# Kernel optimization log

Hardware: AMD Instinct MI355X
Metric: run time of the kernel (lower is better)

Reference implementation:

```python
import jax, jax.numpy as jnp
import numpy as np

N_NODES = 50000
N_EDGES = 600000
N_GRAPHS = 500
IN_DIM = 64
LATENT = [128, 128, 128]
N_CLASSES = 10
N_PROTO_PER_CLASS = 5
N_PROTO = N_CLASSES * N_PROTO_PER_CLASS
GRAPH_SIZE = 10
PROTO_DIM = LATENT[-1]  # single 'mean' readout
EPS = 1e-4


def setup_inputs() -> dict:
    key = jax.random.key(0)
    ks = jax.random.split(key, 12)
    x = jax.random.normal(ks[0], (N_NODES, IN_DIM), dtype=jnp.float32)
    edge_index = jax.random.randint(ks[1], (2, N_EDGES), 0, N_NODES, dtype=jnp.int64)
    batch = jnp.sort(jax.random.randint(ks[2], (N_NODES,), 0, N_GRAPHS, dtype=jnp.int64))
    # GCN layer params (glorot-ish scaling)
    def lin(k, din, dout):
        s = (6.0 / (din + dout)) ** 0.5
        return jax.random.uniform(k, (din, dout), jnp.float32, -s, s)
    W0 = lin(ks[3], IN_DIM, LATENT[0]); b0 = jnp.zeros((LATENT[0],), jnp.float32)
    W1 = lin(ks[4], LATENT[0], LATENT[1]); b1 = jnp.zeros((LATENT[1],), jnp.float32)
    W2 = lin(ks[5], LATENT[1], LATENT[2]); b2 = jnp.zeros((LATENT[2],), jnp.float32)
    s = (6.0 / (GRAPH_SIZE + PROTO_DIM)) ** 0.5
    proto_node_emb = jax.random.uniform(ks[6], (N_PROTO, GRAPH_SIZE, PROTO_DIM), jnp.float32, -s, s)
    # last layer: +1 on correct-class connections, -0.5 on incorrect (set_last_layer_incorrect_connection)
    proto_class = jnp.arange(N_PROTO) // N_PROTO_PER_CLASS  # [P]
    ident = (proto_class[None, :] == jnp.arange(N_CLASSES)[:, None]).astype(jnp.float32)  # [C,P]
    last_w = ident * 1.0 + (1.0 - ident) * (-0.5)
    return {"x": x, "edge_index": edge_index, "batch": batch,
            "W0": W0, "b0": b0, "W1": W1, "b1": b1, "W2": W2, "b2": b2,
            "proto_node_emb": proto_node_emb, "last_w": last_w}


def _gcn_forward(x, edge_index, batch, W0, b0, W1, b1, W2, b2, proto_node_emb, last_w):
    src, dst = edge_index[0], edge_index[1]
    # symmetric normalization with self-loops: deg_i = 1 + in_degree(i)
    deg = 1.0 + jax.ops.segment_sum(jnp.ones((N_EDGES,), jnp.float32), dst, num_segments=N_NODES)
    dis = jax.lax.rsqrt(deg)  # [N]
    norm = dis[src] * dis[dst]  # [E]

    def gcn_layer(h, W, b):
        hw = h @ W  # [N,d]
        agg = jax.ops.segment_sum(hw[src] * norm[:, None], dst, num_segments=N_NODES)
        agg = agg + hw * (dis * dis)[:, None]  # self-loop contribution (norm = 1/deg)
        return agg + b

    h = jax.nn.relu(gcn_layer(x, W0, b0))
    h = jax.nn.relu(gcn_layer(h, W1, b1))
    h = jax.nn.relu(gcn_layer(h, W2, b2))  # node_emb [N, 128]

    # mean readout per graph
    counts = jax.ops.segment_sum(jnp.ones((N_NODES,), jnp.float32), batch, num_segments=N_GRAPHS)
    gsum = jax.ops.segment_sum(h, batch, num_segments=N_GRAPHS)
    graph_emb = gsum / jnp.maximum(counts, 1.0)[:, None]  # [B, 128]

    # prototype graph embeddings via mean readout over prototype nodes
    proto_graph = proto_node_emb.mean(axis=1)  # [P, 128]

    # squared L2 distances [B, P]
    d2 = (jnp.sum(graph_emb ** 2, axis=1)[:, None]
          + jnp.sum(proto_graph ** 2, axis=1)[None, :]
          - 2.0 * graph_emb @ proto_graph.T)
    d2 = jnp.maximum(d2, 0.0)
    sim = jnp.log((d2 + 1.0) / (d2 + EPS))  # [B, P]

    logits = sim @ last_w.T  # [B, C]
    return logits


def reference(x, edge_index, batch, W0, b0, W1, b1, W2, b2, proto_node_emb, last_w):
    return _gcn_forward(x, edge_index, batch, W0, b0, W1, b1, W2, b2, proto_node_emb, last_w)
```

## Files before the change

### kernel.cpp

```cpp
#include <hip/hip_runtime.h>
#include <hip/hip_fp16.h>

#define N_NODES   50000
#define N_EDGES   600000
#define N_GRAPHS  500
#define IN_DIM    64
#define D         128
#define N_CLASSES 10
#define N_PROTO   50
#define GRAPH_SZ  10
#define EPS_F     1e-4f
#define NC4       (N_NODES * IN_DIM / 4)
#define GRP8      ((N_NODES + 7) / 8)
#define G16_TILES (N_NODES / 16)
#define BKT       64
#define NCB       196
#define CBCAP     4096
#define HBLK      392
#define EPB       ((N_EDGES + HBLK - 1) / HBLK)
#define KPT       ((EPB + 255) / 256)

typedef _Float16 half4_t __attribute__((ext_vector_type(4)));
typedef _Float16 half8_t __attribute__((ext_vector_type(8)));
typedef float    f32x4   __attribute__((ext_vector_type(4)));

struct Params {
    const float* x; const int* esrc; const int* edst; const int* bat;
    const float* W0; const float* b0; const float* W1; const float* b1;
    const float* W2; const float* b2; const float* pe; const float* lw;
    float* out;
    _Float16 *bufA, *bufB, *xs, *Bp0, *Bp1, *Bp2;
    float *pg;
    int *src_sorted, *indeg, *coarse, *cursor;
};

__device__ __forceinline__ float dis_of(const int* __restrict__ indeg, int n) {
    return rsqrtf(1.0f + (float)indeg[n]);
}

__device__ __forceinline__ void pack_one(const float* __restrict__ W,
                                         _Float16* __restrict__ Bp, int nks, int t) {
    int j = t & 7, l = (t >> 3) & 63;
    int rest = t >> 9;
    int s = rest % nks, c = rest / nks;
    int k = s * 32 + (l >> 4) * 8 + j;
    int col = c * 16 + (l & 15);
    Bp[t] = (_Float16)W[k * D + col];
}

__global__ void kw_p0(Params P) {
    int i = blockIdx.x * 256 + threadIdx.x;
    if (i < NCB) { P.cursor[i] = 0; return; }
    i -= NCB;
    if (i < 8192)  { pack_one(P.W0, P.Bp0, IN_DIM / 32, i); return; }
    i -= 8192;
    if (i < 16384) { pack_one(P.W1, P.Bp1, D / 32, i); return; }
    i -= 16384;
    if (i < 16384) { pack_one(P.W2, P.Bp2, D / 32, i); return; }
    i -= 16384;
    if (i < N_PROTO * D) {
        int p = i >> 7, j = i & 127;
        float s = 0.f;
#pragma unroll
        for (int g = 0; g < GRAPH_SZ; ++g) s += P.pe[((size_t)p * GRAPH_SZ + g) * D + j];
        P.pg[i] = s * (1.0f / GRAPH_SZ);
        return;
    }
    i -= N_PROTO * D;
    if (i < NC4) {
        float4 v = ((const float4*)P.x)[i];
        half4_t h = { (_Float16)v.x, (_Float16)v.y, (_Float16)v.z, (_Float16)v.w };
        ((half4_t*)P.xs)[i] = h;
    }
}

__global__ __launch_bounds__(256) void kw_hist(Params P) {
    __shared__ int hcnt[NCB];
    __shared__ int hbase[NCB];
    int tid = threadIdx.x;
    for (int i = tid; i < NCB; i += 256) hcnt[i] = 0;
    __syncthreads();
    int e0 = blockIdx.x * EPB;
    int e1 = e0 + EPB; if (e1 > N_EDGES) e1 = N_EDGES;
    int lr[KPT], pb[KPT], pl[KPT];
#pragma unroll
    for (int i = 0; i < KPT; ++i) {
        int e = e0 + i * 256 + tid;
        lr[i] = -1;
        if (e < e1) {
            int d = P.edst[e];
            int b = d >> 8;
            pb[i] = b;
            pl[i] = P.esrc[e] | ((d & 255) << 16);
            lr[i] = atomicAdd(&hcnt[b], 1);
        }
    }
    __syncthreads();
    for (int i = tid; i < NCB; i += 256)
        hbase[i] = hcnt[i] ? atomicAdd(&P.cursor[i], hcnt[i]) : 0;
    __syncthreads();
#pragma unroll
    for (int i = 0; i < KPT; ++i) {
        if (lr[i] >= 0) {
            int pos = hbase[pb[i]] + lr[i];
            if (pos < CBCAP) P.coarse[(pb[i] << 12) + pos] = pl[i];
        }
    }
}

__global__ __launch_bounds__(256) void kw_sort(Params P) {
    __shared__ int edges[CBCAP];
    __shared__ int nrank[256];
    int b = blockIdx.x, tid = threadIdx.x;
    int total = P.cursor[b]; if (total > CBCAP) total = CBCAP;
    for (int i = tid; i < total; i += 256) edges[i] = P.coarse[(b << 12) + i];
    nrank[tid] = 0;
    __syncthreads();
    for (int i = tid; i < total; i += 256) {
        int pl = edges[i];
        int dl = pl >> 16;
        int r = atomicAdd(&nrank[dl], 1);
        if (r < BKT) P.src_sorted[(((b << 8) | dl) << 6) + r] = pl & 0xFFFF;
    }
    __syncthreads();
    int node = (b << 8) + tid;
    if (node < N_NODES) P.indeg[node] = nrank[tid];
}

__global__ __launch_bounds__(256, 8) void kw_a0g01(Params P) {
    __shared__ _Float16 xa_t[16][72];
    __shared__ _Float16 h1_t[16][136];
    int tid = threadIdx.x;
    int row0 = blockIdx.x * 16;
    int grp = tid >> 5, lane16 = tid & 15, hf = (tid >> 4) & 1;
    int j4 = lane16 * 4;

#pragma unroll
    for (int iter = 0; iter < 2; ++iter) {
        int nrel = iter * 8 + grp;
        int node = row0 + nrel;
        int cnt = P.indeg[node];
        int base = node << 6;
        float a0 = 0.f, a1 = 0.f, a2 = 0.f, a3 = 0.f;
        int k = hf;
        if (k < cnt) {
            int sc = P.src_sorted[base + k];
            float dc = dis_of(P.indeg, sc);
            half4_t vc = *(const half4_t*)&P.xs[(size_t)sc * IN_DIM + j4];
            for (k += 2; k < cnt; k += 2) {
                int sn = P.src_sorted[base + k];
                float dn = dis_of(P.indeg, sn);
                half4_t vn = *(const half4_t*)&P.xs[(size_t)sn * IN_DIM + j4];
                a0 = fmaf((float)vc[0], dc, a0);
                a1 = fmaf((float)vc[1], dc, a1);
                a2 = fmaf((float)vc[2], dc, a2);
                a3 = fmaf((float)vc[3], dc, a3);
                vc = vn; dc = dn;
            }
            a0 = fmaf((float)vc[0], dc, a0);
            a1 = fmaf((float)vc[1], dc, a1);
            a2 = fmaf((float)vc[2], dc, a2);
            a3 = fmaf((float)vc[3], dc, a3);
        }
        a0 += __shfl_xor(a0, 16);
        a1 += __shfl_xor(a1, 16);
        a2 += __shfl_xor(a2, 16);
        a3 += __shfl_xor(a3, 16);
        if (hf == 0) {
            half4_t hv = *(const half4_t*)&P.xs[(size_t)node * IN_DIM + j4];
            float dd = rsqrtf(1.0f + (float)cnt);
            half4_t r = { (_Float16)((fmaf((float)hv[0], dd, a0)) * dd),
                          (_Float16)((fmaf((float)hv[1], dd, a1)) * dd),
                          (_Float16)((fmaf((float)hv[2], dd, a2)) * dd),
                          (_Float16)((fmaf((float)hv[3], dd, a3)) * dd) };
            *(half4_t*)&xa_t[nrel][j4] = r;
        }
    }
    __syncthreads();

    int wave = tid >> 6, lane = tid & 63;
    int l15 = lane & 15;
    int kof = (lane >> 4) * 8;
    int rb  = (lane >> 4) * 4;
    {
        half8_t af0 = *(const half8_t*)&xa_t[l15][kof];
        half8_t af1 = *(const half8_t*)&xa_t[l15][32 + kof];
        f32x4 acc[2];
        acc[0] = (f32x4){0.f, 0.f, 0.f, 0.f};
        acc[1] = (f32x4){0.f, 0.f, 0.f, 0.f};
#pragma unroll
        for (int cc = 0; cc < 2; ++cc) {
            int c = wave * 2 + cc;
            half8_t b0f = *(const half8_t*)&P.Bp0[(size_t)((c * 2 + 0) * 64 + lane) * 8];
            half8_t b1f = *(const half8_t*)&P.Bp0[(size_t)((c * 2 + 1) * 64 + lane) * 8];
            acc[cc] = __builtin_amdgcn_mfma_f32_16x16x32_f16(af0, b0f, acc[cc], 0, 0, 0);
            acc[cc] = __builtin_amdgcn_mfma_f32_16x16x32_f16(af1, b1f, acc[cc], 0, 0, 0);
        }
#pragma unroll
        for (int cc = 0; cc < 2; ++cc) {
            int col = (wave * 2 + cc) * 16 + l15;
            float bv = P.b0[col];
#pragma unroll
            for (int r = 0; r < 4; ++r)
                h1_t[rb + r][col] = (_Float16)fmaxf(acc[cc][r] + bv, 0.f);
        }
    }
    __syncthreads();

    {
        half8_t af[4];
#pragma unroll
        for (int s = 0; s < 4; ++s)
            af[s] = *(const half8_t*)&h1_t[l15][s * 32 + kof];
        f32x4 acc[2];
        acc[0] = (f32x4){0.f, 0.f, 0.f, 0.f};
        acc[1] = (f32x4){0.f, 0.f, 0.f, 0.f};
#pragma unroll
        for (int cc = 0; cc < 2; ++cc) {
            int c = wave * 2 + cc;
#pragma unroll
            for (int s = 0; s < 4; ++s) {
                half8_t bf = *(const half8_t*)&P.Bp1[(size_t)((c * 4 + s) * 64 + lane) * 8];
                acc[cc] = __builtin_amdgcn_mfma_f32_16x16x32_f16(af[s], bf, acc[cc], 0, 0, 0);
            }
        }
        float dsc[4];
#pragma unroll
        for (int r = 0; r < 4; ++r) dsc[r] = dis_of(P.indeg, row0 + rb + r);
#pragma unroll
        for (int cc = 0; cc < 2; ++cc) {
            int col = (wave * 2 + cc) * 16 + l15;
#pragma unroll
            for (int r = 0; r < 4; ++r)
                P.bufA[(size_t)(row0 + rb + r) * D + col] = (_Float16)(acc[cc][r] * dsc[r]);
        }
    }
}

__global__ __launch_bounds__(256, 8) void kw_g1g2(Params P) {
    __shared__ _Float16 h2_t[16][136];
    int tid = threadIdx.x;
    int row0 = blockIdx.x * 16;
    int grp = tid >> 5, lane16 = tid & 15, hf = (tid >> 4) & 1;
    int j8 = lane16 * 8;

#pragma unroll
    for (int iter = 0; iter < 2; ++iter) {
        int nrel = iter * 8 + grp;
        int node = row0 + nrel;
        int cnt = P.indeg[node];
        int base = node << 6;
        float a[8] = {0.f, 0.f, 0.f, 0.f, 0.f, 0.f, 0.f, 0.f};
        int k = hf;
        if (k < cnt) {
            int sc = P.src_sorted[base + k];
            half8_t vc = *(const half8_t*)&P.bufA[(size_t)sc * D + j8];
            for (k += 2; k < cnt; k += 2) {
                int sn = P.src_sorted[base + k];
                half8_t vn = *(const half8_t*)&P.bufA[(size_t)sn * D + j8];
#pragma unroll
                for (int j = 0; j < 8; ++j) a[j] += (float)vc[j];
                vc = vn;
            }
#pragma unroll
            for (int j = 0; j < 8; ++j) a[j] += (float)vc[j];
        }
#pragma unroll
        for (int j = 0; j < 8; ++j) a[j] += __shfl_xor(a[j], 16);
        if (hf == 0) {
            float dd = rsqrtf(1.0f + (float)cnt);
            half8_t hv = *(const half8_t*)&P.bufA[(size_t)node * D + j8];
            half8_t r;
#pragma unroll
            for (int j = 0; j < 8; ++j)
                r[j] = (_Float16)fmaxf((a[j] + (float)hv[j]) * dd + P.b1[j8 + j], 0.f);
            *(half8_t*)&h2_t[nrel][j8] = r;
        }
    }
    __syncthreads();

    int wave = tid >> 6, lane = tid & 63;
    int l15 = lane & 15;
    int kof = (lane >> 4) * 8;
    int rb  = (lane >> 4) * 4;
    half8_t af[4];
#pragma unroll
    for (int s = 0; s < 4; ++s)
        af[s] = *(const half8_t*)&h2_t[l15][s * 32 + kof];
    f32x4 acc[2];
    acc[0] = (f32x4){0.f, 0.f, 0.f, 0.f};
    acc[1] = (f32x4){0.f, 0.f, 0.f, 0.f};
#pragma unroll
    for (int cc = 0; cc < 2; ++cc) {
        int c = wave * 2 + cc;
#pragma unroll
        for (int s = 0; s < 4; ++s) {
            half8_t bf = *(const half8_t*)&P.Bp2[(size_t)((c * 4 + s) * 64 + lane) * 8];
            acc[cc] = __builtin_amdgcn_mfma_f32_16x16x32_f16(af[s], bf, acc[cc], 0, 0, 0);
        }
    }
    float dsc[4];
#pragma unroll
    for (int r = 0; r < 4; ++r) dsc[r] = dis_of(P.indeg, row0 + rb + r);
#pragma unroll
    for (int cc = 0; cc < 2; ++cc) {
        int col = (wave * 2 + cc) * 16 + l15;
#pragma unroll
        for (int r = 0; r < 4; ++r)
            P.bufB[(size_t)(row0 + rb + r) * D + col] = (_Float16)(acc[cc][r] * dsc[r]);
    }
}

__global__ __launch_bounds__(256, 8) void kw_gather2(Params P) {
    int node = blockIdx.x * 8 + (threadIdx.x >> 5);
    if (node >= N_NODES) return;
    int lane16 = threadIdx.x & 15;
    int hf = (threadIdx.x >> 4) & 1;
    int j8 = lane16 * 8;
    int cnt = P.indeg[node];
    int base = node << 6;
    float a[8] = {0.f, 0.f, 0.f, 0.f, 0.f, 0.f, 0.f, 0.f};
    int k = hf;
    if (k < cnt) {
        int sc = P.src_sorted[base + k];
        half8_t vc = *(const half8_t*)&P.bufB[(size_t)sc * D + j8];
        for (k += 2; k < cnt; k += 2) {
            int sn = P.src_sorted[base + k];
            half8_t vn = *(const half8_t*)&P.bufB[(size_t)sn * D + j8];
#pragma unroll
            for (int j = 0; j < 8; ++j) a[j] += (float)vc[j];
            vc = vn;
        }
#pragma unroll
        for (int j = 0; j < 8; ++j) a[j] += (float)vc[j];
    }
#pragma unroll
    for (int j = 0; j < 8; ++j) a[j] += __shfl_xor(a[j], 16);
    if (hf == 0) {
        float dd = rsqrtf(1.0f + (float)cnt);
        half8_t hv = *(const half8_t*)&P.bufB[(size_t)node * D + j8];
        half8_t r;
#pragma unroll
        for (int j = 0; j < 8; ++j)
            r[j] = (_Float16)fmaxf((a[j] + (float)hv[j]) * dd + P.b2[j8 + j], 0.f);
        *(half8_t*)&P.bufA[(size_t)node * D + j8] = r;
    }
}

__global__ void kw_readout(Params P) {
    __shared__ int sh[2];
    __shared__ float red[4][D];
    __shared__ float gs[D];
    __shared__ float sim[N_PROTO];
    const _Float16* h = P.bufA;
    int g = blockIdx.x;
    if (threadIdx.x == 0) {
        int lo = 0, hi = N_NODES;
        while (lo < hi) { int m = (lo + hi) >> 1; if (P.bat[m] < g) lo = m + 1; else hi = m; }
        sh[0] = lo;
        hi = N_NODES;
        while (lo < hi) { int m = (lo + hi) >> 1; if (P.bat[m] < g + 1) lo = m + 1; else hi = m; }
        sh[1] = lo;
    }
    __syncthreads();
    int s0 = sh[0], s1 = sh[1];
    int col = threadIdx.x & 127;
    int part = threadIdx.x >> 7;
    float sum = 0.f;
    for (int n = s0 + part; n < s1; n += 4) sum += (float)h[(size_t)n * D + col];
    red[part][col] = sum;
    __syncthreads();
    if (part == 0)
        gs[col] = (sum + red[1][col] + red[2][col] + red[3][col])
                  / fmaxf((float)(s1 - s0), 1.0f);
    __syncthreads();
    int t = threadIdx.x;
    if (t < N_PROTO * 8) {
        int p = t >> 3, sub = t & 7;
        const float* q = P.pg + (size_t)p * D;
        float d2 = 0.f;
        int j0 = sub * 16;
#pragma unroll
        for (int j = 0; j < 16; ++j) {
            float df = gs[j0 + j] - q[j0 + j];
            d2 = fmaf(df, df, d2);
        }
        d2 += __shfl_xor(d2, 1);
        d2 += __shfl_xor(d2, 2);
        d2 += __shfl_xor(d2, 4);
        if (sub == 0) sim[p] = logf((d2 + 1.0f) / (d2 + EPS_F));
    }
    __syncthreads();
    if (t < N_CLASSES) {
        float s = 0.f;
#pragma unroll
        for (int p = 0; p < N_PROTO; ++p) s = fmaf(sim[p], P.lw[t * N_PROTO + p], s);
        P.out[(size_t)g * N_CLASSES + t] = s;
    }
}

extern "C" void kernel_launch(void* const* d_in, const int* in_sizes, int n_in,
                              void* d_out, int out_size, void* d_ws, size_t ws_size,
                              hipStream_t stream) {
    Params P;
    P.x    = (const float*)d_in[0];
    P.esrc = (const int*)d_in[1];
    P.edst = (const int*)d_in[1] + N_EDGES;
    P.bat  = (const int*)d_in[2];
    P.W0 = (const float*)d_in[3];  P.b0 = (const float*)d_in[4];
    P.W1 = (const float*)d_in[5];  P.b1 = (const float*)d_in[6];
    P.W2 = (const float*)d_in[7];  P.b2 = (const float*)d_in[8];
    P.pe = (const float*)d_in[9];  P.lw = (const float*)d_in[10];
    P.out = (float*)d_out;

    char* wsb = (char*)d_ws;
    P.bufA = (_Float16*)wsb;  wsb += (size_t)N_NODES * D * 2;
    P.bufB = (_Float16*)wsb;  wsb += (size_t)N_NODES * D * 2;
    P.xs   = (_Float16*)wsb;  wsb += (size_t)N_NODES * IN_DIM * 2;
    P.Bp0  = (_Float16*)wsb;  wsb += (size_t)IN_DIM * D * 2;
    P.Bp1  = (_Float16*)wsb;  wsb += (size_t)D * D * 2;
    P.Bp2  = (_Float16*)wsb;  wsb += (size_t)D * D * 2;
    P.pg   = (float*)wsb;     wsb += (size_t)N_PROTO * D * 4;
    P.src_sorted = (int*)wsb; wsb += (size_t)N_NODES * BKT * 4;
    P.coarse     = (int*)wsb; wsb += (size_t)NCB * CBCAP * 4;
    P.indeg      = (int*)wsb; wsb += (size_t)N_NODES * 4;
    P.cursor     = (int*)wsb; wsb += (size_t)NCB * 4;

    const int TB = 256;
    int p0_threads = NCB + 8192 + 16384 + 16384 + N_PROTO * D + NC4;
    int p0_blocks  = (p0_threads + TB - 1) / TB;

    kw_p0<<<p0_blocks, TB, 0, stream>>>(P);
    kw_hist<<<HBLK, TB, 0, stream>>>(P);
    kw_sort<<<NCB, TB, 0, stream>>>(P);
    kw_a0g01<<<G16_TILES, TB, 0, stream>>>(P);
    kw_g1g2<<<G16_TILES, TB, 0, stream>>>(P);
    kw_gather2<<<GRP8, TB, 0, stream>>>(P);
    kw_readout<<<N_GRAPHS, 512, 0, stream>>>(P);
}
```

Measured before the change: 134.6 us.

## Fuse mean-readout sum into final gather and move x conversion into hist kernel

The final GCN gather kernel now accumulates ReLU outputs per graph in shared memory and atomically adds them into a global per-graph sum buffer, instead of writing node embeddings for a separate readout pass to reread. The readout kernel becomes a small finish kernel that divides by counts and computes distances and logits. The fp32-to-fp16 conversion of x moves from the first kernel into extra blocks of the histogram kernel so it overlaps with edge bucketing. The cost is float atomics, which make summation order nondeterministic.

```diff
diff --git a/kernel.cpp b/kernel.cpp
--- a/kernel.cpp
+++ b/kernel.cpp
@@ -19,6 +19,7 @@
 #define HBLK      392
 #define EPB       ((N_EDGES + HBLK - 1) / HBLK)
 #define KPT       ((EPB + 255) / 256)
+#define CONV_BLK  ((NC4 + 255) / 256)
 
 typedef _Float16 half4_t __attribute__((ext_vector_type(4)));
 typedef _Float16 half8_t __attribute__((ext_vector_type(8)));
@@ -30,7 +31,7 @@
     const float* W2; const float* b2; const float* pe; const float* lw;
     float* out;
     _Float16 *bufA, *bufB, *xs, *Bp0, *Bp1, *Bp2;
-    float *pg;
+    float *pg, *gsum;
     int *src_sorted, *indeg, *coarse, *cursor;
 };
 
@@ -52,6 +53,8 @@
     int i = blockIdx.x * 256 + threadIdx.x;
     if (i < NCB) { P.cursor[i] = 0; return; }
     i -= NCB;
+    if (i < N_GRAPHS * D) { P.gsum[i] = 0.f; return; }
+    i -= N_GRAPHS * D;
     if (i < 8192)  { pack_one(P.W0, P.Bp0, IN_DIM / 32, i); return; }
     i -= 8192;
     if (i < 16384) { pack_one(P.W1, P.Bp1, D / 32, i); return; }
@@ -64,17 +67,19 @@
 #pragma unroll
         for (int g = 0; g < GRAPH_SZ; ++g) s += P.pe[((size_t)p * GRAPH_SZ + g) * D + j];
         P.pg[i] = s * (1.0f / GRAPH_SZ);
+    }
+}
+
+__global__ __launch_bounds__(256) void kw_hist(Params P) {
+    if (blockIdx.x >= HBLK) {
+        int i = (blockIdx.x - HBLK) * 256 + threadIdx.x;
+        if (i < NC4) {
+            float4 v = ((const float4*)P.x)[i];
+            half4_t h = { (_Float16)v.x, (_Float16)v.y, (_Float16)v.z, (_Float16)v.w };
+            ((half4_t*)P.xs)[i] = h;
+        }
         return;
     }
-    i -= N_PROTO * D;
-    if (i < NC4) {
-        float4 v = ((const float4*)P.x)[i];
-        half4_t h = { (_Float16)v.x, (_Float16)v.y, (_Float16)v.z, (_Float16)v.w };
-        ((half4_t*)P.xs)[i] = h;
-    }
-}
-
-__global__ __launch_bounds__(256) void kw_hist(Params P) {
     __shared__ int hcnt[NCB];
     __shared__ int hbase[NCB];
     int tid = threadIdx.x;
@@ -311,12 +316,19 @@
     }
 }
 
-__global__ __launch_bounds__(256, 8) void kw_gather2(Params P) {
-    int node = blockIdx.x * 8 + (threadIdx.x >> 5);
-    if (node >= N_NODES) return;
-    int lane16 = threadIdx.x & 15;
-    int hf = (threadIdx.x >> 4) & 1;
+__global__ __launch_bounds__(256, 8) void kw_g2r(Params P) {
+    __shared__ float part[8][D];
+    __shared__ int sg0;
+    int tid = threadIdx.x;
+    int n0 = blockIdx.x * 8;
+    int node = n0 + (tid >> 5);
+    int lane16 = tid & 15;
+    int hf = (tid >> 4) & 1;
     int j8 = lane16 * 8;
+    for (int i = tid; i < 8 * D; i += 256) ((float*)part)[i] = 0.f;
+    if (tid == 0) sg0 = P.bat[n0];
+    __syncthreads();
+
     int cnt = P.indeg[node];
     int base = node << 6;
     float a[8] = {0.f, 0.f, 0.f, 0.f, 0.f, 0.f, 0.f, 0.f};
@@ -339,20 +351,33 @@
     if (hf == 0) {
         float dd = rsqrtf(1.0f + (float)cnt);
         half8_t hv = *(const half8_t*)&P.bufB[(size_t)node * D + j8];
-        half8_t r;
+        float v[8];
 #pragma unroll
         for (int j = 0; j < 8; ++j)
-            r[j] = (_Float16)fmaxf((a[j] + (float)hv[j]) * dd + P.b2[j8 + j], 0.f);
-        *(half8_t*)&P.bufA[(size_t)node * D + j8] = r;
-    }
-}
-
-__global__ void kw_readout(Params P) {
+            v[j] = fmaxf((a[j] + (float)hv[j]) * dd + P.b2[j8 + j], 0.f);
+        int g = P.bat[node];
+        int gi = g - sg0;
+        if (gi < 8) {
+#pragma unroll
+            for (int j = 0; j < 8; ++j) atomicAdd(&part[gi][j8 + j], v[j]);
+        } else {
+#pragma unroll
+            for (int j = 0; j < 8; ++j) atomicAdd(&P.gsum[(size_t)g * D + j8 + j], v[j]);
+        }
+    }
+    __syncthreads();
+    int gspan = P.bat[n0 + 7] - sg0 + 1;
+    if (gspan > 8) gspan = 8;
+    for (int i = tid; i < gspan * D; i += 256) {
+        float v = ((float*)part)[i];
+        if (v != 0.f) atomicAdd(&P.gsum[(size_t)(sg0 + (i >> 7)) * D + (i & 127)], v);
+    }
+}
+
+__global__ void kw_finish(Params P) {
     __shared__ int sh[2];
-    __shared__ float red[4][D];
     __shared__ float gs[D];
     __shared__ float sim[N_PROTO];
-    const _Float16* h = P.bufA;
     int g = blockIdx.x;
     if (threadIdx.x == 0) {
         int lo = 0, hi = N_NODES;
@@ -363,16 +388,8 @@
         sh[1] = lo;
     }
     __syncthreads();
-    int s0 = sh[0], s1 = sh[1];
-    int col = threadIdx.x & 127;
-    int part = threadIdx.x >> 7;
-    float sum = 0.f;
-    for (int n = s0 + part; n < s1; n += 4) sum += (float)h[(size_t)n * D + col];
-    red[part][col] = sum;
-    __syncthreads();
-    if (part == 0)
-        gs[col] = (sum + red[1][col] + red[2][col] + red[3][col])
-                  / fmaxf((float)(s1 - s0), 1.0f);
+    float cnt = fmaxf((float)(sh[1] - sh[0]), 1.0f);
+    if (threadIdx.x < D) gs[threadIdx.x] = P.gsum[(size_t)g * D + threadIdx.x] / cnt;
     __syncthreads();
     int t = threadIdx.x;
     if (t < N_PROTO * 8) {
@@ -421,20 +438,21 @@
     P.Bp1  = (_Float16*)wsb;  wsb += (size_t)D * D * 2;
     P.Bp2  = (_Float16*)wsb;  wsb += (size_t)D * D * 2;
     P.pg   = (float*)wsb;     wsb += (size_t)N_PROTO * D * 4;
+    P.gsum = (float*)wsb;     wsb += (size_t)N_GRAPHS * D * 4;
     P.src_sorted = (int*)wsb; wsb += (size_t)N_NODES * BKT * 4;
     P.coarse     = (int*)wsb; wsb += (size_t)NCB * CBCAP * 4;
     P.indeg      = (int*)wsb; wsb += (size_t)N_NODES * 4;
     P.cursor     = (int*)wsb; wsb += (size_t)NCB * 4;
 
     const int TB = 256;
-    int p0_threads = NCB + 8192 + 16384 + 16384 + N_PROTO * D + NC4;
+    int p0_threads = NCB + N_GRAPHS * D + 8192 + 16384 + 16384 + N_PROTO * D;
     int p0_blocks  = (p0_threads + TB - 1) / TB;
 
     kw_p0<<<p0_blocks, TB, 0, stream>>>(P);
-    kw_hist<<<HBLK, TB, 0, stream>>>(P);
+    kw_hist<<<HBLK + CONV_BLK, TB, 0, stream>>>(P);
     kw_sort<<<NCB, TB, 0, stream>>>(P);
     kw_a0g01<<<G16_TILES, TB, 0, stream>>>(P);
     kw_g1g2<<<G16_TILES, TB, 0, stream>>>(P);
-    kw_gather2<<<GRP8, TB, 0, stream>>>(P);
-    kw_readout<<<N_GRAPHS, 512, 0, stream>>>(P);
-}
+    kw_g2r<<<GRP8, TB, 0, stream>>>(P);
+    kw_finish<<<N_GRAPHS, 512, 0, stream>>>(P);
+}
```

After: 154.5 us. 1.15x slower.
